# Kernel tuning notes

Measured on AMD Instinct MI355X. Metric: run time of the kernel, lower is better.

The kernel has to match this reference:

```python
import jax, jax.numpy as jnp
import numpy as np

N = 50000
E = 800000
F_IN = 64
HID = 64


def setup_inputs() -> dict:
    key = jax.random.key(0)
    k1, k2, k3, k4, k5, k6 = jax.random.split(key, 6)
    x = jax.random.normal(k1, (N, F_IN), dtype=jnp.float32)
    edge_index = jax.random.randint(k2, (2, E), 0, N, dtype=jnp.int64)
    # GraphSAGE mean-aggregator layers: Linear(2*in -> out) applied to [x || mean_agg(x)]
    W1 = jax.random.normal(k3, (2 * F_IN, HID), dtype=jnp.float32) / np.sqrt(2 * F_IN)
    b1 = jnp.zeros((HID,), dtype=jnp.float32)
    W2 = jax.random.normal(k4, (2 * HID, HID), dtype=jnp.float32) / np.sqrt(2 * HID)
    b2 = jnp.zeros((HID,), dtype=jnp.float32)
    return {"x": x, "edge_index": edge_index, "W1": W1, "b1": b1, "W2": W2, "b2": b2}


def _sage_conv(x, src, dst, W, b):
    # mean aggregation of neighbor (src) features at dst, then linear on [self || agg]
    msg = x[src]                                                   # [E, d] gather
    s = jax.ops.segment_sum(msg, dst, num_segments=N)              # [N, d]
    cnt = jax.ops.segment_sum(jnp.ones((src.shape[0], 1), x.dtype), dst, num_segments=N)
    agg = s / jnp.maximum(cnt, 1.0)
    return jnp.concatenate([x, agg], axis=-1) @ W + b


def reference(x, edge_index, W1, b1, W2, b2):
    src, dst = edge_index[0], edge_index[1]
    h = _sage_conv(x, src, dst, W1, b1)
    h = jax.nn.relu(h)  # dropout is identity at inference
    h = _sage_conv(h, src, dst, W2, b2)
    return h
```

## Files before the change

### kernel.cpp

```cpp
#include <hip/hip_runtime.h>

#define N_NODES 50000
#define N_EDGES 800000
#define F 64
#define CHUNK 3072
#define NWG1 ((N_EDGES + CHUNK - 1) / CHUNK)
#define NBUCK 196
#define BSTRIDE 8192
#define NWTILE (N_NODES / 16)

typedef __attribute__((ext_vector_type(8))) _Float16 half8;
typedef __attribute__((ext_vector_type(4))) float f32x4;

__global__ __launch_bounds__(256) void partition_conv(
    const int*    __restrict__ src, const int* __restrict__ dst,
    const float4* __restrict__ xin,
    half8*        __restrict__ x16,
    const float*  __restrict__ W1, const float* __restrict__ W2,
    _Float16*     __restrict__ Wt1, _Float16* __restrict__ Wt2,
    unsigned*     __restrict__ bcur,
    unsigned*     __restrict__ ebuf) {
  int t = threadIdx.x, b = blockIdx.x;
  if (b == NWG1) {
    for (int i = t; i < 64 * 128; i += 256) {
      int n = i >> 7, k = i & 127;
      Wt1[i] = (_Float16)W1[k * 64 + n];
      Wt2[i] = (_Float16)W2[k * 64 + n];
    }
    return;
  }
  __shared__ int hist[256], lscan[256], lcur[256], gbase[256];
  __shared__ unsigned stage[CHUNK];
  hist[t] = 0; __syncthreads();
  int e0 = b * CHUNK;
  int cnt = N_EDGES - e0; if (cnt > CHUNK) cnt = CHUNK;
  for (int i = t; i < cnt; i += 256) atomicAdd(&hist[dst[e0 + i] >> 8], 1);

  const int TOT = N_NODES * F / 8;
  for (int i = b * 256 + t; i < TOT; i += NWG1 * 256) {
    float4 a = xin[i * 2], c = xin[i * 2 + 1];
    half8 hh;
    hh[0] = (_Float16)a.x; hh[1] = (_Float16)a.y;
    hh[2] = (_Float16)a.z; hh[3] = (_Float16)a.w;
    hh[4] = (_Float16)c.x; hh[5] = (_Float16)c.y;
    hh[6] = (_Float16)c.z; hh[7] = (_Float16)c.w;
    x16[i] = hh;
  }
  __syncthreads();

  int v = hist[t];
  lscan[t] = v; __syncthreads();
  for (int off = 1; off < 256; off <<= 1) {
    int a = (t >= off) ? lscan[t - off] : 0;
    __syncthreads();
    lscan[t] += a;
    __syncthreads();
  }
  lscan[t] -= v;
  lcur[t] = lscan[t];
  if (v > 0) gbase[t] = (int)atomicAdd(&bcur[t], (unsigned)v);
  __syncthreads();

  for (int i = t; i < cnt; i += 256) {
    int d = dst[e0 + i], s = src[e0 + i];
    int bb = d >> 8;
    int p = atomicAdd(&lcur[bb], 1);
    stage[p] = ((unsigned)bb << 24) | ((unsigned)(d & 255) << 16) | (unsigned)s;
  }
  __syncthreads();
  for (int i = t; i < cnt; i += 256) {
    unsigned e = stage[i];
    int bb = e >> 24;
    ebuf[bb * BSTRIDE + gbase[bb] + (i - lscan[bb])] = e;
  }
}

__global__ __launch_bounds__(256) void bucket_sort(
    const unsigned* __restrict__ ebuf, const unsigned* __restrict__ bcur,
    unsigned short* __restrict__ edge_src, int* __restrict__ row_start,
    int* __restrict__ deg) {
  __shared__ int lhist[128], lscan[128], lcur[128];
  __shared__ unsigned short srt[BSTRIDE / 2];
  int B = blockIdx.x, t = threadIdx.x;
  int b = B >> 1, h = B & 1;
  int s0 = b * BSTRIDE;
  int cnt = (int)bcur[b];

  if (t < 128) lhist[t] = 0;
  __syncthreads();
  for (int i = t; i < cnt; i += 256) {
    int bin = (int)((ebuf[s0 + i] >> 16) & 255);
    if ((bin >> 7) == h) atomicAdd(&lhist[bin & 127], 1);
  }
  __syncthreads();

  int v = (t < 128) ? lhist[t] : 0;
  if (t < 128) lscan[t] = v;
  __syncthreads();
  for (int off = 1; off < 128; off <<= 1) {
    int a = (t >= off && t < 128) ? lscan[t - off] : 0;
    __syncthreads();
    if (t < 128) lscan[t] += a;
    __syncthreads();
  }
  if (t < 128) { lscan[t] -= v; lcur[t] = lscan[t]; }
  __syncthreads();

  int total = lscan[127] + lhist[127];
  int base  = h ? (cnt - total) : 0;

  for (int i = t; i < cnt; i += 256) {
    unsigned e = ebuf[s0 + i];
    int bin = (int)((e >> 16) & 255);
    if ((bin >> 7) == h) {
      int p = atomicAdd(&lcur[bin & 127], 1);
      srt[p] = (unsigned short)(e & 0xFFFFu);
    }
  }
  __syncthreads();

  for (int i = t; i < total; i += 256) edge_src[s0 + base + i] = srt[i];

  if (t < 128) {
    int n = b * 256 + h * 128 + t;
    if (n < N_NODES) { row_start[n] = s0 + base + lscan[t]; deg[n] = v; }
  }
}

__global__ __launch_bounds__(256) void sage_layer_fused(
    const half8*    __restrict__ feat16,
    const _Float16* __restrict__ self16,
    const int*      __restrict__ row_start,
    const int*      __restrict__ deg,
    const unsigned short* __restrict__ edge_src,
    const _Float16* __restrict__ Wt,
    const float*    __restrict__ bias,
    float*          __restrict__ outf,
    unsigned short* __restrict__ out16,
    int do_relu) {
  __shared__ _Float16 lmean[32 * 72];
  int t = threadIdx.x;
  int w = t >> 6, lane = t & 63;

  {
    int o = lane >> 3, q = lane & 7;
    int n = blockIdx.x * 32 + w * 8 + o;
    if (n < N_NODES) {
      int start = row_start[n];
      int d     = deg[n];
      half8 acc8 = (half8){0, 0, 0, 0, 0, 0, 0, 0};
      for (int base = 0; base < d; base += 8) {
        #pragma unroll
        for (int uu = 0; uu < 8; ++uu) {
          int e = base + uu;
          if (e < d) {
            int s = (int)edge_src[start + e];
            acc8 += feat16[(size_t)s * 8 + q];
          }
        }
      }
      float inv = (d > 0) ? 1.0f / (float)d : 0.0f;
      half8 h;
      #pragma unroll
      for (int k = 0; k < 8; ++k) h[k] = (_Float16)((float)acc8[k] * inv);
      *(half8*)&lmean[(w * 8 + o) * 72 + q * 8] = h;
    }
  }
  __syncthreads();

  int tile = w >> 1;
  int wt = blockIdx.x * 2 + tile;
  if (wt >= NWTILE) return;
  int m = lane & 15, quad = lane >> 4;
  size_t arow = (size_t)(wt * 16 + m) * 64 + quad * 8;
  half8 a0 = *(const half8*)(self16 + arow);
  half8 a1 = *(const half8*)(self16 + arow + 32);
  int ln = tile * 16 + m;
  half8 a2 = *(const half8*)&lmean[ln * 72 + quad * 8];
  half8 a3 = *(const half8*)&lmean[ln * 72 + quad * 8 + 32];

  int nt0 = (w & 1) * 2;
  #pragma unroll
  for (int i = 0; i < 2; ++i) {
    int nt = nt0 + i;
    float bv = bias[nt * 16 + m];
    f32x4 acc = (f32x4){bv, bv, bv, bv};
    const _Float16* wrow = Wt + (size_t)(nt * 16 + m) * 128 + quad * 8;
    half8 b0 = *(const half8*)(wrow);
    half8 b1 = *(const half8*)(wrow + 32);
    half8 b2 = *(const half8*)(wrow + 64);
    half8 b3 = *(const half8*)(wrow + 96);
    acc = __builtin_amdgcn_mfma_f32_16x16x32_f16(a0, b0, acc, 0, 0, 0);
    acc = __builtin_amdgcn_mfma_f32_16x16x32_f16(a1, b1, acc, 0, 0, 0);
    acc = __builtin_amdgcn_mfma_f32_16x16x32_f16(a2, b2, acc, 0, 0, 0);
    acc = __builtin_amdgcn_mfma_f32_16x16x32_f16(a3, b3, acc, 0, 0, 0);
    #pragma unroll
    for (int r = 0; r < 4; ++r) {
      size_t off = (size_t)(wt * 16 + quad * 4 + r) * 64 + nt * 16 + m;
      float v = acc[r];
      if (do_relu) v = fmaxf(v, 0.0f);
      if (outf)  outf[off] = v;
      if (out16) { _Float16 hv = (_Float16)v; out16[off] = *(unsigned short*)&hv; }
    }
  }
}

extern "C" void kernel_launch(void* const* d_in, const int* in_sizes, int n_in,
                              void* d_out, int out_size, void* d_ws, size_t ws_size,
                              hipStream_t stream) {
  const float* x  = (const float*)d_in[0];
  const int*   ei = (const int*)d_in[1];
  const float* W1 = (const float*)d_in[2];
  const float* b1 = (const float*)d_in[3];
  const float* W2 = (const float*)d_in[4];
  const float* b2 = (const float*)d_in[5];
  float* out = (float*)d_out;

  const int* src = ei;
  const int* dst = ei + N_EDGES;

  int* wsi       = (int*)d_ws;
  unsigned* bcur = (unsigned*)wsi;
  int* deg       = wsi + 256;
  int* row_start = wsi + 50304;
  unsigned short* edge_src = (unsigned short*)(wsi + 100352);
  unsigned* ebuf = (unsigned*)(wsi + 903168);
  half8* x16     = (half8*)(wsi + 2508800);
  unsigned short* h116 = (unsigned short*)(wsi + 4108800);
  _Float16* Wt1  = (_Float16*)(wsi + 5708800);
  _Float16* Wt2  = (_Float16*)(wsi + 5712896);

  hipMemsetAsync(bcur, 0, 256 * sizeof(unsigned), stream);

  dim3 blk(256);
  partition_conv<<<NWG1 + 1, blk, 0, stream>>>(
      src, dst, (const float4*)x, x16, W1, W2, Wt1, Wt2, bcur, ebuf);
  bucket_sort<<<NBUCK * 2, blk, 0, stream>>>(ebuf, bcur, edge_src, row_start, deg);

  dim3 grd_fused((N_NODES + 31) / 32);

  sage_layer_fused<<<grd_fused, blk, 0, stream>>>(
      x16, (const _Float16*)x16, row_start, deg, edge_src,
      Wt1, b1, nullptr, h116, 1);
  sage_layer_fused<<<grd_fused, blk, 0, stream>>>(
      (const half8*)h116, (const _Float16*)h116, row_start, deg, edge_src,
      Wt2, b2, out, nullptr, 0);
}
```

Baseline: 159.8 us.

## Pad per-node edge lists to 8 and gather neighbors in unconditional batches of 16

The bucket sort now pads each node's source list to a multiple of 8 with zero indices and gives each half-bucket a fixed half-stride base, so row starts are 16-byte aligned. The aggregation loop loads 16 neighbor indices as two vector loads and prefetches the next batch. It issues all 16 feature gathers unconditionally and masks only the accumulation. The goal is more memory-level parallelism and fewer scalar index loads in the gather. The cost is extra, wasted gathers for low-degree nodes, and reads of indices past the padded data, which may be uninitialised memory and point outside the feature array.

```diff
diff --git a/kernel.cpp b/kernel.cpp
--- a/kernel.cpp
+++ b/kernel.cpp
@@ -11,6 +11,7 @@
 
 typedef __attribute__((ext_vector_type(8))) _Float16 half8;
 typedef __attribute__((ext_vector_type(4))) float f32x4;
+typedef __attribute__((ext_vector_type(8))) unsigned short ushort8v;
 
 __global__ __launch_bounds__(256) void partition_conv(
     const int*    __restrict__ src, const int* __restrict__ dst,
@@ -94,8 +95,9 @@
   }
   __syncthreads();
 
-  int v = (t < 128) ? lhist[t] : 0;
-  if (t < 128) lscan[t] = v;
+  int v  = (t < 128) ? lhist[t] : 0;
+  int pv = (v + 7) & ~7;
+  if (t < 128) lscan[t] = pv;
   __syncthreads();
   for (int off = 1; off < 128; off <<= 1) {
     int a = (t >= off && t < 128) ? lscan[t - off] : 0;
@@ -103,11 +105,11 @@
     if (t < 128) lscan[t] += a;
     __syncthreads();
   }
-  if (t < 128) { lscan[t] -= v; lcur[t] = lscan[t]; }
-  __syncthreads();
-
-  int total = lscan[127] + lhist[127];
-  int base  = h ? (cnt - total) : 0;
+  if (t < 128) { lscan[t] -= pv; lcur[t] = lscan[t]; }
+  __syncthreads();
+
+  int total_p = lscan[127] + ((lhist[127] + 7) & ~7);
+  int base    = h * (BSTRIDE / 2);
 
   for (int i = t; i < cnt; i += 256) {
     unsigned e = ebuf[s0 + i];
@@ -118,8 +120,13 @@
     }
   }
   __syncthreads();
-
-  for (int i = t; i < total; i += 256) edge_src[s0 + base + i] = srt[i];
+  if (t < 128) {
+    int p0 = lscan[t];
+    for (int j = v; j < pv; ++j) srt[p0 + j] = 0;
+  }
+  __syncthreads();
+
+  for (int i = t; i < total_p; i += 256) edge_src[s0 + base + i] = srt[i];
 
   if (t < 128) {
     int n = b * 256 + h * 128 + t;
@@ -149,21 +156,64 @@
       int start = row_start[n];
       int d     = deg[n];
       half8 acc8 = (half8){0, 0, 0, 0, 0, 0, 0, 0};
-      for (int base = 0; base < d; base += 8) {
-        #pragma unroll
-        for (int uu = 0; uu < 8; ++uu) {
-          int e = base + uu;
-          if (e < d) {
-            int s = (int)edge_src[start + e];
-            acc8 += feat16[(size_t)s * 8 + q];
+      if (d > 0) {
+        const ushort8v* idp = (const ushort8v*)(edge_src + start);
+        int nb = (d + 15) >> 4;
+        ushort8v iA = idp[0], iB = idp[1];
+        for (int b = 0; b < nb; ++b) {
+          half8 h0 = feat16[(size_t)iA[0] * 8 + q];
+          half8 h1 = feat16[(size_t)iA[1] * 8 + q];
+          half8 h2 = feat16[(size_t)iA[2] * 8 + q];
+          half8 h3 = feat16[(size_t)iA[3] * 8 + q];
+          half8 h4 = feat16[(size_t)iA[4] * 8 + q];
+          half8 h5 = feat16[(size_t)iA[5] * 8 + q];
+          half8 h6 = feat16[(size_t)iA[6] * 8 + q];
+          half8 h7 = feat16[(size_t)iA[7] * 8 + q];
+          half8 h8 = feat16[(size_t)iB[0] * 8 + q];
+          half8 h9 = feat16[(size_t)iB[1] * 8 + q];
+          half8 hA = feat16[(size_t)iB[2] * 8 + q];
+          half8 hB = feat16[(size_t)iB[3] * 8 + q];
+          half8 hC = feat16[(size_t)iB[4] * 8 + q];
+          half8 hD = feat16[(size_t)iB[5] * 8 + q];
+          half8 hE = feat16[(size_t)iB[6] * 8 + q];
+          half8 hF = feat16[(size_t)iB[7] * 8 + q];
+          ushort8v nA, nB;
+          if (b + 1 < nb) {
+            nA = idp[2 * b + 2];
+            nB = idp[2 * b + 3];
           }
+          int b0 = b * 16;
+          if (b0 + 16 <= d) {
+            acc8 += h0; acc8 += h1; acc8 += h2; acc8 += h3;
+            acc8 += h4; acc8 += h5; acc8 += h6; acc8 += h7;
+            acc8 += h8; acc8 += h9; acc8 += hA; acc8 += hB;
+            acc8 += hC; acc8 += hD; acc8 += hE; acc8 += hF;
+          } else {
+            if (b0 +  0 < d) acc8 += h0;
+            if (b0 +  1 < d) acc8 += h1;
+            if (b0 +  2 < d) acc8 += h2;
+            if (b0 +  3 < d) acc8 += h3;
+            if (b0 +  4 < d) acc8 += h4;
+            if (b0 +  5 < d) acc8 += h5;
+            if (b0 +  6 < d) acc8 += h6;
+            if (b0 +  7 < d) acc8 += h7;
+            if (b0 +  8 < d) acc8 += h8;
+            if (b0 +  9 < d) acc8 += h9;
+            if (b0 + 10 < d) acc8 += hA;
+            if (b0 + 11 < d) acc8 += hB;
+            if (b0 + 12 < d) acc8 += hC;
+            if (b0 + 13 < d) acc8 += hD;
+            if (b0 + 14 < d) acc8 += hE;
+            if (b0 + 15 < d) acc8 += hF;
+          }
+          if (b + 1 < nb) { iA = nA; iB = nB; }
         }
       }
       float inv = (d > 0) ? 1.0f / (float)d : 0.0f;
-      half8 h;
+      half8 hm;
       #pragma unroll
-      for (int k = 0; k < 8; ++k) h[k] = (_Float16)((float)acc8[k] * inv);
-      *(half8*)&lmean[(w * 8 + o) * 72 + q * 8] = h;
+      for (int k = 0; k < 8; ++k) hm[k] = (_Float16)((float)acc8[k] * inv);
+      *(half8*)&lmean[(w * 8 + o) * 72 + q * 8] = hm;
     }
   }
   __syncthreads();
```

Result: faster. 148.3 us (-7.2%).

## Pad neighbor lists to 16 with sentinel row and software-pipeline gathers

Applied to the files above, without the earlier changes.

Each node's neighbor list in the bucket sort is padded to a multiple of 16 using a sentinel node index whose feature row is zeroed, so the gather loop no longer needs per-edge bounds checks. The aggregation loop loads indices as 8-wide vectors and double-buffers two batches of 8 feature gathers, issuing the next batch before accumulating the current one to keep more memory requests in flight. Launch bounds are raised to target 4 blocks per SM. In exchange, padding adds wasted sentinel gathers for low-degree nodes, and many live half8 registers risk spilling or lower occupancy. Each half-bucket is also assumed to fit in BSTRIDE/2 entries after padding.

```diff
diff --git a/kernel.cpp b/kernel.cpp
--- a/kernel.cpp
+++ b/kernel.cpp
@@ -8,14 +8,17 @@
 #define NBUCK 196
 #define BSTRIDE 8192
 #define NWTILE (N_NODES / 16)
+#define NSENT N_NODES
 
 typedef __attribute__((ext_vector_type(8))) _Float16 half8;
 typedef __attribute__((ext_vector_type(4))) float f32x4;
+typedef __attribute__((ext_vector_type(8))) unsigned short ushort8v;
 
 __global__ __launch_bounds__(256) void partition_conv(
     const int*    __restrict__ src, const int* __restrict__ dst,
     const float4* __restrict__ xin,
     half8*        __restrict__ x16,
+    unsigned short* __restrict__ h116,
     const float*  __restrict__ W1, const float* __restrict__ W2,
     _Float16*     __restrict__ Wt1, _Float16* __restrict__ Wt2,
     unsigned*     __restrict__ bcur,
@@ -27,6 +30,8 @@
       Wt1[i] = (_Float16)W1[k * 64 + n];
       Wt2[i] = (_Float16)W2[k * 64 + n];
     }
+    if (t < 32) ((unsigned*)(x16 + (size_t)NSENT * 8))[t] = 0;
+    if (t >= 64 && t < 96) ((unsigned*)h116)[(size_t)NSENT * 32 + (t - 64)] = 0;
     return;
   }
   __shared__ int hist[256], lscan[256], lcur[256], gbase[256];
@@ -94,8 +99,9 @@
   }
   __syncthreads();
 
-  int v = (t < 128) ? lhist[t] : 0;
-  if (t < 128) lscan[t] = v;
+  int v  = (t < 128) ? lhist[t] : 0;
+  int pv = (v + 15) & ~15;
+  if (t < 128) lscan[t] = pv;
   __syncthreads();
   for (int off = 1; off < 128; off <<= 1) {
     int a = (t >= off && t < 128) ? lscan[t - off] : 0;
@@ -103,11 +109,11 @@
     if (t < 128) lscan[t] += a;
     __syncthreads();
   }
-  if (t < 128) { lscan[t] -= v; lcur[t] = lscan[t]; }
-  __syncthreads();
-
-  int total = lscan[127] + lhist[127];
-  int base  = h ? (cnt - total) : 0;
+  if (t < 128) { lscan[t] -= pv; lcur[t] = lscan[t]; }
+  __syncthreads();
+
+  int total_p = lscan[127] + ((lhist[127] + 15) & ~15);
+  int base    = h * (BSTRIDE / 2);
 
   for (int i = t; i < cnt; i += 256) {
     unsigned e = ebuf[s0 + i];
@@ -118,8 +124,13 @@
     }
   }
   __syncthreads();
-
-  for (int i = t; i < total; i += 256) edge_src[s0 + base + i] = srt[i];
+  if (t < 128) {
+    int p0 = lscan[t];
+    for (int j = v; j < pv; ++j) srt[p0 + j] = (unsigned short)NSENT;
+  }
+  __syncthreads();
+
+  for (int i = t; i < total_p; i += 256) edge_src[s0 + base + i] = srt[i];
 
   if (t < 128) {
     int n = b * 256 + h * 128 + t;
@@ -127,7 +138,7 @@
   }
 }
 
-__global__ __launch_bounds__(256) void sage_layer_fused(
+__global__ __launch_bounds__(256, 4) void sage_layer_fused(
     const half8*    __restrict__ feat16,
     const _Float16* __restrict__ self16,
     const int*      __restrict__ row_start,
@@ -149,21 +160,64 @@
       int start = row_start[n];
       int d     = deg[n];
       half8 acc8 = (half8){0, 0, 0, 0, 0, 0, 0, 0};
-      for (int base = 0; base < d; base += 8) {
-        #pragma unroll
-        for (int uu = 0; uu < 8; ++uu) {
-          int e = base + uu;
-          if (e < d) {
-            int s = (int)edge_src[start + e];
-            acc8 += feat16[(size_t)s * 8 + q];
+      if (d > 0) {
+        const ushort8v* idp = (const ushort8v*)(edge_src + start);
+        int nb2 = (d + 15) >> 4;
+        ushort8v iA = idp[0], iB = idp[1];
+        half8 a0 = feat16[(size_t)iA[0] * 8 + q];
+        half8 a1 = feat16[(size_t)iA[1] * 8 + q];
+        half8 a2 = feat16[(size_t)iA[2] * 8 + q];
+        half8 a3 = feat16[(size_t)iA[3] * 8 + q];
+        half8 a4 = feat16[(size_t)iA[4] * 8 + q];
+        half8 a5 = feat16[(size_t)iA[5] * 8 + q];
+        half8 a6 = feat16[(size_t)iA[6] * 8 + q];
+        half8 a7 = feat16[(size_t)iA[7] * 8 + q];
+        half8 e0 = feat16[(size_t)iB[0] * 8 + q];
+        half8 e1 = feat16[(size_t)iB[1] * 8 + q];
+        half8 e2 = feat16[(size_t)iB[2] * 8 + q];
+        half8 e3 = feat16[(size_t)iB[3] * 8 + q];
+        half8 e4 = feat16[(size_t)iB[4] * 8 + q];
+        half8 e5 = feat16[(size_t)iB[5] * 8 + q];
+        half8 e6 = feat16[(size_t)iB[6] * 8 + q];
+        half8 e7 = feat16[(size_t)iB[7] * 8 + q];
+        for (int p = 0; ; ++p) {
+          bool more = (p + 1 < nb2);
+          ushort8v nA, nB;
+          if (more) { nA = idp[2 * p + 2]; nB = idp[2 * p + 3]; }
+          acc8 += a0; acc8 += a1; acc8 += a2; acc8 += a3;
+          acc8 += a4; acc8 += a5; acc8 += a6; acc8 += a7;
+          if (more) {
+            iA = nA;
+            a0 = feat16[(size_t)iA[0] * 8 + q];
+            a1 = feat16[(size_t)iA[1] * 8 + q];
+            a2 = feat16[(size_t)iA[2] * 8 + q];
+            a3 = feat16[(size_t)iA[3] * 8 + q];
+            a4 = feat16[(size_t)iA[4] * 8 + q];
+            a5 = feat16[(size_t)iA[5] * 8 + q];
+            a6 = feat16[(size_t)iA[6] * 8 + q];
+            a7 = feat16[(size_t)iA[7] * 8 + q];
           }
+          acc8 += e0; acc8 += e1; acc8 += e2; acc8 += e3;
+          acc8 += e4; acc8 += e5; acc8 += e6; acc8 += e7;
+          if (more) {
+            iB = nB;
+            e0 = feat16[(size_t)iB[0] * 8 + q];
+            e1 = feat16[(size_t)iB[1] * 8 + q];
+            e2 = feat16[(size_t)iB[2] * 8 + q];
+            e3 = feat16[(size_t)iB[3] * 8 + q];
+            e4 = feat16[(size_t)iB[4] * 8 + q];
+            e5 = feat16[(size_t)iB[5] * 8 + q];
+            e6 = feat16[(size_t)iB[6] * 8 + q];
+            e7 = feat16[(size_t)iB[7] * 8 + q];
+          }
+          if (!more) break;
         }
       }
       float inv = (d > 0) ? 1.0f / (float)d : 0.0f;
-      half8 h;
+      half8 hm;
       #pragma unroll
-      for (int k = 0; k < 8; ++k) h[k] = (_Float16)((float)acc8[k] * inv);
-      *(half8*)&lmean[(w * 8 + o) * 72 + q * 8] = h;
+      for (int k = 0; k < 8; ++k) hm[k] = (_Float16)((float)acc8[k] * inv);
+      *(half8*)&lmean[(w * 8 + o) * 72 + q * 8] = hm;
     }
   }
   __syncthreads();
@@ -226,15 +280,15 @@
   unsigned short* edge_src = (unsigned short*)(wsi + 100352);
   unsigned* ebuf = (unsigned*)(wsi + 903168);
   half8* x16     = (half8*)(wsi + 2508800);
-  unsigned short* h116 = (unsigned short*)(wsi + 4108800);
-  _Float16* Wt1  = (_Float16*)(wsi + 5708800);
-  _Float16* Wt2  = (_Float16*)(wsi + 5712896);
+  unsigned short* h116 = (unsigned short*)(wsi + 4109312);
+  _Float16* Wt1  = (_Float16*)(wsi + 5709824);
+  _Float16* Wt2  = (_Float16*)(wsi + 5713920);
 
   hipMemsetAsync(bcur, 0, 256 * sizeof(unsigned), stream);
 
   dim3 blk(256);
   partition_conv<<<NWG1 + 1, blk, 0, stream>>>(
-      src, dst, (const float4*)x, x16, W1, W2, Wt1, Wt2, bcur, ebuf);
+      src, dst, (const float4*)x, x16, h116, W1, W2, Wt1, Wt2, bcur, ebuf);
   bucket_sort<<<NBUCK * 2, blk, 0, stream>>>(ebuf, bcur, edge_src, row_start, deg);
 
   dim3 grd_fused((N_NODES + 31) / 32);
```

Result: faster. 149.8 us (-6.2%).

## Split aggregation from linear, pad edge lists with sentinel for vectorized gathers

Applied to the files above, without the earlier changes.

Per-node edge lists are padded to multiples of 16 with a sentinel index pointing at a zeroed feature row. This lets the aggregation kernel load eight indices at once and issue eight independent gathers per iteration, with no per-edge bounds checks. Aggregation and the MFMA linear step become separate kernels, with mean features going through global memory. The aggregation kernel gets an occupancy hint of 8 blocks. The cost is two extra launches per forward pass and an extra round-trip of the mean buffer through global memory.

```diff
diff --git a/kernel.cpp b/kernel.cpp
--- a/kernel.cpp
+++ b/kernel.cpp
@@ -8,14 +8,17 @@
 #define NBUCK 196
 #define BSTRIDE 8192
 #define NWTILE (N_NODES / 16)
+#define NSENT N_NODES
 
 typedef __attribute__((ext_vector_type(8))) _Float16 half8;
 typedef __attribute__((ext_vector_type(4))) float f32x4;
+typedef __attribute__((ext_vector_type(8))) unsigned short ushort8v;
 
 __global__ __launch_bounds__(256) void partition_conv(
     const int*    __restrict__ src, const int* __restrict__ dst,
     const float4* __restrict__ xin,
     half8*        __restrict__ x16,
+    unsigned short* __restrict__ h116,
     const float*  __restrict__ W1, const float* __restrict__ W2,
     _Float16*     __restrict__ Wt1, _Float16* __restrict__ Wt2,
     unsigned*     __restrict__ bcur,
@@ -27,6 +30,8 @@
       Wt1[i] = (_Float16)W1[k * 64 + n];
       Wt2[i] = (_Float16)W2[k * 64 + n];
     }
+    if (t < 32) ((unsigned*)(x16 + (size_t)NSENT * 8))[t] = 0;
+    if (t >= 64 && t < 96) ((unsigned*)h116)[(size_t)NSENT * 32 + (t - 64)] = 0;
     return;
   }
   __shared__ int hist[256], lscan[256], lcur[256], gbase[256];
@@ -94,8 +99,9 @@
   }
   __syncthreads();
 
-  int v = (t < 128) ? lhist[t] : 0;
-  if (t < 128) lscan[t] = v;
+  int v  = (t < 128) ? lhist[t] : 0;
+  int pv = (v + 15) & ~15;
+  if (t < 128) lscan[t] = pv;
   __syncthreads();
   for (int off = 1; off < 128; off <<= 1) {
     int a = (t >= off && t < 128) ? lscan[t - off] : 0;
@@ -103,11 +109,11 @@
     if (t < 128) lscan[t] += a;
     __syncthreads();
   }
-  if (t < 128) { lscan[t] -= v; lcur[t] = lscan[t]; }
-  __syncthreads();
-
-  int total = lscan[127] + lhist[127];
-  int base  = h ? (cnt - total) : 0;
+  if (t < 128) { lscan[t] -= pv; lcur[t] = lscan[t]; }
+  __syncthreads();
+
+  int total_p = lscan[127] + ((lhist[127] + 15) & ~15);
+  int base    = h * (BSTRIDE / 2);
 
   for (int i = t; i < cnt; i += 256) {
     unsigned e = ebuf[s0 + i];
@@ -118,8 +124,13 @@
     }
   }
   __syncthreads();
-
-  for (int i = t; i < total; i += 256) edge_src[s0 + base + i] = srt[i];
+  if (t < 128) {
+    int p0 = lscan[t];
+    for (int j = v; j < pv; ++j) srt[p0 + j] = (unsigned short)NSENT;
+  }
+  __syncthreads();
+
+  for (int i = t; i < total_p; i += 256) edge_src[s0 + base + i] = srt[i];
 
   if (t < 128) {
     int n = b * 256 + h * 128 + t;
@@ -127,62 +138,70 @@
   }
 }
 
-__global__ __launch_bounds__(256) void sage_layer_fused(
+__global__ __launch_bounds__(256, 8) void sage_aggregate(
     const half8*    __restrict__ feat16,
-    const _Float16* __restrict__ self16,
     const int*      __restrict__ row_start,
     const int*      __restrict__ deg,
     const unsigned short* __restrict__ edge_src,
+    half8*          __restrict__ mean16) {
+  int t = threadIdx.x;
+  int w = t >> 6, lane = t & 63;
+  int o = lane >> 3, q = lane & 7;
+  int n = blockIdx.x * 32 + w * 8 + o;
+  if (n >= N_NODES) return;
+  int start = row_start[n];
+  int d     = deg[n];
+  half8 acc8 = (half8){0, 0, 0, 0, 0, 0, 0, 0};
+  if (d > 0) {
+    const ushort8v* idp = (const ushort8v*)(edge_src + start);
+    int nb = ((d + 15) & ~15) >> 3;
+    ushort8v iv = idp[0];
+    for (int b = 0; b < nb; ++b) {
+      half8 h0 = feat16[(size_t)iv[0] * 8 + q];
+      half8 h1 = feat16[(size_t)iv[1] * 8 + q];
+      half8 h2 = feat16[(size_t)iv[2] * 8 + q];
+      half8 h3 = feat16[(size_t)iv[3] * 8 + q];
+      half8 h4 = feat16[(size_t)iv[4] * 8 + q];
+      half8 h5 = feat16[(size_t)iv[5] * 8 + q];
+      half8 h6 = feat16[(size_t)iv[6] * 8 + q];
+      half8 h7 = feat16[(size_t)iv[7] * 8 + q];
+      ushort8v nv;
+      bool more = (b + 1 < nb);
+      if (more) nv = idp[b + 1];
+      acc8 += h0; acc8 += h1; acc8 += h2; acc8 += h3;
+      acc8 += h4; acc8 += h5; acc8 += h6; acc8 += h7;
+      if (more) iv = nv;
+    }
+  }
+  float inv = (d > 0) ? 1.0f / (float)d : 0.0f;
+  half8 hm;
+  #pragma unroll
+  for (int k = 0; k < 8; ++k) hm[k] = (_Float16)((float)acc8[k] * inv);
+  mean16[(size_t)n * 8 + q] = hm;
+}
+
+__global__ __launch_bounds__(256) void sage_linear(
+    const _Float16* __restrict__ self16,
+    const half8*    __restrict__ mean16,
     const _Float16* __restrict__ Wt,
     const float*    __restrict__ bias,
     float*          __restrict__ outf,
     unsigned short* __restrict__ out16,
     int do_relu) {
-  __shared__ _Float16 lmean[32 * 72];
   int t = threadIdx.x;
   int w = t >> 6, lane = t & 63;
-
-  {
-    int o = lane >> 3, q = lane & 7;
-    int n = blockIdx.x * 32 + w * 8 + o;
-    if (n < N_NODES) {
-      int start = row_start[n];
-      int d     = deg[n];
-      half8 acc8 = (half8){0, 0, 0, 0, 0, 0, 0, 0};
-      for (int base = 0; base < d; base += 8) {
-        #pragma unroll
-        for (int uu = 0; uu < 8; ++uu) {
-          int e = base + uu;
-          if (e < d) {
-            int s = (int)edge_src[start + e];
-            acc8 += feat16[(size_t)s * 8 + q];
-          }
-        }
-      }
-      float inv = (d > 0) ? 1.0f / (float)d : 0.0f;
-      half8 h;
-      #pragma unroll
-      for (int k = 0; k < 8; ++k) h[k] = (_Float16)((float)acc8[k] * inv);
-      *(half8*)&lmean[(w * 8 + o) * 72 + q * 8] = h;
-    }
-  }
-  __syncthreads();
-
-  int tile = w >> 1;
-  int wt = blockIdx.x * 2 + tile;
+  int wt = blockIdx.x * 4 + w;
   if (wt >= NWTILE) return;
   int m = lane & 15, quad = lane >> 4;
   size_t arow = (size_t)(wt * 16 + m) * 64 + quad * 8;
   half8 a0 = *(const half8*)(self16 + arow);
   half8 a1 = *(const half8*)(self16 + arow + 32);
-  int ln = tile * 16 + m;
-  half8 a2 = *(const half8*)&lmean[ln * 72 + quad * 8];
-  half8 a3 = *(const half8*)&lmean[ln * 72 + quad * 8 + 32];
-
-  int nt0 = (w & 1) * 2;
+  size_t mrow = (size_t)(wt * 16 + m) * 8;
+  half8 a2 = mean16[mrow + quad];
+  half8 a3 = mean16[mrow + quad + 4];
+
   #pragma unroll
-  for (int i = 0; i < 2; ++i) {
-    int nt = nt0 + i;
+  for (int nt = 0; nt < 4; ++nt) {
     float bv = bias[nt * 16 + m];
     f32x4 acc = (f32x4){bv, bv, bv, bv};
     const _Float16* wrow = Wt + (size_t)(nt * 16 + m) * 128 + quad * 8;
@@ -226,23 +245,26 @@
   unsigned short* edge_src = (unsigned short*)(wsi + 100352);
   unsigned* ebuf = (unsigned*)(wsi + 903168);
   half8* x16     = (half8*)(wsi + 2508800);
-  unsigned short* h116 = (unsigned short*)(wsi + 4108800);
-  _Float16* Wt1  = (_Float16*)(wsi + 5708800);
-  _Float16* Wt2  = (_Float16*)(wsi + 5712896);
+  unsigned short* h116 = (unsigned short*)(wsi + 4109312);
+  _Float16* Wt1  = (_Float16*)(wsi + 5709824);
+  _Float16* Wt2  = (_Float16*)(wsi + 5713920);
+  half8* mean16  = (half8*)(wsi + 5718016);
 
   hipMemsetAsync(bcur, 0, 256 * sizeof(unsigned), stream);
 
   dim3 blk(256);
   partition_conv<<<NWG1 + 1, blk, 0, stream>>>(
-      src, dst, (const float4*)x, x16, W1, W2, Wt1, Wt2, bcur, ebuf);
+      src, dst, (const float4*)x, x16, h116, W1, W2, Wt1, Wt2, bcur, ebuf);
   bucket_sort<<<NBUCK * 2, blk, 0, stream>>>(ebuf, bcur, edge_src, row_start, deg);
 
-  dim3 grd_fused((N_NODES + 31) / 32);
-
-  sage_layer_fused<<<grd_fused, blk, 0, stream>>>(
-      x16, (const _Float16*)x16, row_start, deg, edge_src,
-      Wt1, b1, nullptr, h116, 1);
-  sage_layer_fused<<<grd_fused, blk, 0, stream>>>(
-      (const half8*)h116, (const _Float16*)h116, row_start, deg, edge_src,
-      Wt2, b2, out, nullptr, 0);
-}
+  dim3 grd_agg((N_NODES + 31) / 32);
+  dim3 grd_lin((NWTILE + 3) / 4);
+
+  sage_aggregate<<<grd_agg, blk, 0, stream>>>(x16, row_start, deg, edge_src, mean16);
+  sage_linear<<<grd_lin, blk, 0, stream>>>((const _Float16*)x16, mean16,
+                                           Wt1, b1, nullptr, h116, 1);
+  sage_aggregate<<<grd_agg, blk, 0, stream>>>((const half8*)h116, row_start, deg,
+                                              edge_src, mean16);
+  sage_linear<<<grd_lin, blk, 0, stream>>>((const _Float16*)h116, mean16,
+                                           Wt2, b2, out, nullptr, 0);
+}
```

Measured after the change: 157.2 us. No clear change (-1.7%).
